# Kernel optimization log

Measured on AMD Instinct MI355X. Metric: run time of the kernel, lower is better.

## Reference

```python
import jax, jax.numpy as jnp
import numpy as np

GROUPS = 4
CHANNELS = 512
SCALE = 0.02


def setup_inputs() -> dict:
    key = jax.random.key(0)
    k_x, k_w1, k_w2, k_b1, k_b2 = jax.random.split(key, 5)
    d = CHANNELS // GROUPS
    x = jax.random.normal(k_x, (8, CHANNELS, 128, 128), dtype=jnp.float32)
    w1 = SCALE * jax.random.normal(k_w1, (2, GROUPS, d, d), dtype=jnp.float32)
    w2 = SCALE * jax.random.normal(k_w2, (2, GROUPS, d, d), dtype=jnp.float32)
    b1 = SCALE * jax.random.normal(k_b1, (2, GROUPS, d), dtype=jnp.float32)
    b2 = SCALE * jax.random.normal(k_b2, (2, GROUPS, d), dtype=jnp.float32)
    return {"x": x, "w1": w1, "w2": w2, "b1": b1, "b2": b2}


def reference(x, w1, w2, b1, b2):
    B, C, H, W = x.shape
    g = w1.shape[1]
    d = C // g
    # FFT over spatial dims; spectrum [B, C, H, W//2+1] complex
    spec = jnp.fft.rfft2(x, axes=(2, 3), norm="ortho")
    origin = spec
    out = spec.reshape(B, g, d, H, spec.shape[-1])  # B (g d) H Wf -> B g d H Wf
    xr, xi = out.real, out.imag

    def cmul(ar, ai, w, b):
        # grouped complex matmul over channel dim + bias
        or_ = (jnp.einsum("bkihw,kio->bkohw", ar, w[0])
               - jnp.einsum("bkihw,kio->bkohw", ai, w[1])
               + b[0][None, :, :, None, None])
        oi_ = (jnp.einsum("bkihw,kio->bkohw", ai, w[0])
               + jnp.einsum("bkihw,kio->bkohw", ar, w[1])
               + b[1][None, :, :, None, None])
        return or_, oi_

    o1r, o1i = cmul(xr, xi, w1, b1)
    o1r, o1i = jax.nn.relu(o1r), jax.nn.relu(o1i)
    o2r, o2i = cmul(o1r, o1i, w2, b2)

    out_c = (o2r + 1j * o2i).reshape(B, C, H, spec.shape[-1])
    out_c = out_c * origin
    return jnp.fft.irfft2(out_c, s=(H, W), axes=(2, 3), norm="ortho")
```

## Files before the change

kernel.cpp:

```cpp
#include <hip/hip_runtime.h>
#include <hip/hip_bf16.h>


#define NB    8
#define NC    512
#define NG    4
#define ND    128
#define NH    128
#define NW    128
#define NWF   65
#define NM    (NWF * NH)
#define INV_N 0.0078125f

typedef unsigned short ushortT;
typedef unsigned int uintT;
typedef __bf16 bf16x8 __attribute__((ext_vector_type(8)));
typedef float f32x4 __attribute__((ext_vector_type(4)));

__device__ __forceinline__ ushortT f2b(float f) {
    __hip_bfloat16 h = __float2bfloat16(f);
    return __builtin_bit_cast(ushortT, h);
}

__device__ __forceinline__ uintT pk2(float a, float b) {
    return (uintT)f2b(a) | ((uintT)f2b(b) << 16);
}
__device__ __forceinline__ float lo2f(uintT u) {
    return __builtin_bit_cast(float, u << 16);
}
__device__ __forceinline__ float hi2f(uintT u) {
    return __builtin_bit_cast(float, u & 0xffff0000u);
}

__device__ __forceinline__ int sigma(int n) {
    return ((n & 15) << 4) | ((n >> 4) & 7) | ((n & 128) >> 4);
}

__device__ __forceinline__ int bitrev7(int x) {
    return (int)(__brev((unsigned)x) >> 25);
}

__device__ __forceinline__ int IDX(int r, int c) {
    return (r << 7) + (c ^ (r & 15));
}

__device__ __forceinline__ float2 cmul(float2 a, float2 b) {
    return make_float2(a.x * b.x - a.y * b.y, a.x * b.y + a.y * b.x);
}

template <bool INV>
__device__ __forceinline__ void r4pass(float2* D, const float2* __restrict__ twg,
                                       int tid, int s) {
    const int h = 1 << s;
#pragma unroll
    for (int t = 0; t < 2; t++) {
        const int idx = t * 1024 + tid;
        const int rlo = idx & 15;
        const int gid = (idx >> 4) & 31;
        const int r = ((idx >> 9) << 4) | rlo;
        const int j = gid & (h - 1);
        const int base = ((gid >> s) << (s + 2)) + j;
        float2 t2 = twg[j << (5 - s)];
        float2 t1 = twg[j << (6 - s)];
        if (INV) { t1.y = -t1.y; t2.y = -t2.y; }
        float2 a = D[IDX(r, base)];
        float2 b = D[IDX(r, base + h)];
        float2 c = D[IDX(r, base + 2 * h)];
        float2 d = D[IDX(r, base + 3 * h)];
        float2 tb = cmul(t1, b), td = cmul(t1, d);
        float2 a1 = make_float2(a.x + tb.x, a.y + tb.y);
        float2 b1 = make_float2(a.x - tb.x, a.y - tb.y);
        float2 c1 = make_float2(c.x + td.x, c.y + td.y);
        float2 d1 = make_float2(c.x - td.x, c.y - td.y);
        float2 tc = cmul(t2, c1), ud = cmul(t2, d1);
        float2 rot = INV ? make_float2(-ud.y, ud.x) : make_float2(ud.y, -ud.x);
        D[IDX(r, base)]         = make_float2(a1.x + tc.x, a1.y + tc.y);
        D[IDX(r, base + h)]     = make_float2(b1.x + rot.x, b1.y + rot.y);
        D[IDX(r, base + 2 * h)] = make_float2(a1.x - tc.x, a1.y - tc.y);
        D[IDX(r, base + 3 * h)] = make_float2(b1.x - rot.x, b1.y - rot.y);
    }
    __syncthreads();
}

template <bool INV>
__device__ __forceinline__ void r2final(float2* D, const float2* __restrict__ twg,
                                        int tid) {
#pragma unroll
    for (int t = 0; t < 4; t++) {
        const int idx = t * 1024 + tid;
        const int rlo = idx & 15;
        const int j = (idx >> 4) & 63;
        const int r = ((idx >> 10) << 4) | rlo;
        float2 w = twg[j];
        if (INV) w.y = -w.y;
        float2 xl = D[IDX(r, j)];
        float2 xh = D[IDX(r, j + 64)];
        const float tr = w.x * xh.x - w.y * xh.y;
        const float ti = w.x * xh.y + w.y * xh.x;
        D[IDX(r, j)]      = make_float2(xl.x + tr, xl.y + ti);
        D[IDX(r, j + 64)] = make_float2(xl.x - tr, xl.y - ti);
    }
    __syncthreads();
}

template <bool INV>
__device__ __forceinline__ void fft64x128(float2* D, const float2* __restrict__ twg,
                                          int tid) {
    r4pass<INV>(D, twg, tid, 0);
    r4pass<INV>(D, twg, tid, 2);
    r4pass<INV>(D, twg, tid, 4);
    r2final<INV>(D, twg, tid);
}

__global__ __launch_bounds__(1024, 8) void k_fwd2d(const float* __restrict__ x,
                                                   uintT* __restrict__ s0,
                                                   const float2* __restrict__ twg) {
    __shared__ float2 D[8192];
    const int tid = threadIdx.x;
    const int bc = blockIdx.x;

    const float* xr = x + (size_t)bc * (NH * NW);
#pragma unroll
    for (int t = 0; t < 2; t++) {
        int i = t * 1024 + tid;
        int hp = i >> 5;
        int w0 = (i & 31) * 4;
        float4 a = *(const float4*)(xr + (size_t)(2 * hp) * NW + w0);
        float4 b = *(const float4*)(xr + (size_t)(2 * hp + 1) * NW + w0);
        D[IDX(hp, bitrev7(w0 + 0))] = make_float2(a.x, b.x);
        D[IDX(hp, bitrev7(w0 + 1))] = make_float2(a.y, b.y);
        D[IDX(hp, bitrev7(w0 + 2))] = make_float2(a.z, b.z);
        D[IDX(hp, bitrev7(w0 + 3))] = make_float2(a.w, b.w);
    }
    __syncthreads();
    fft64x128<false>(D, twg, tid);

    float2 ra[4], rb[4];
#pragma unroll
    for (int t = 0; t < 4; t++) {
        int i = t * 1024 + tid;
        int hp = i >> 6, j = i & 63;
        ra[t] = D[IDX(hp, j)];
        rb[t] = D[IDX(hp, j ? (128 - j) : 64)];
    }
    __syncthreads();
#pragma unroll
    for (int t = 0; t < 4; t++) {
        int i = t * 1024 + tid;
        int hp = i >> 6, j = i & 63;
        int c0 = bitrev7(2 * hp), c1 = bitrev7(2 * hp + 1);
        float2 a = ra[t], b = rb[t];
        if (j == 0) {
            D[IDX(0, c0)] = make_float2(a.x, b.x);
            D[IDX(0, c1)] = make_float2(a.y, b.y);
        } else {
            D[IDX(j, c0)] = make_float2(0.5f * (a.x + b.x), 0.5f * (a.y - b.y));
            D[IDX(j, c1)] = make_float2(0.5f * (a.y + b.y), 0.5f * (b.x - a.x));
        }
    }
    __syncthreads();
    fft64x128<false>(D, twg, tid);

    uintT* o = s0 + (size_t)bc * NM;
#pragma unroll
    for (int t = 0; t < 8; t++) {
        int i = t * 1024 + tid;
        int r = i >> 7, k = i & 127;
        if (r) {
            float2 v = D[IDX(r, k)];
            o[r * 128 + k] = pk2(v.x * INV_N, v.y * INV_N);
        } else {
            float2 ck = D[IDX(0, k)];
            float2 cm = D[IDX(0, (128 - k) & 127)];
            o[k] = pk2(0.5f * (ck.x + cm.x) * INV_N,
                       0.5f * (ck.y - cm.y) * INV_N);
            o[64 * 128 + k] = pk2(0.5f * (ck.y + cm.y) * INV_N,
                                  0.5f * (cm.x - ck.x) * INV_N);
        }
    }
}

__global__ __launch_bounds__(1024, 8) void k_inv2d(const uintT* __restrict__ y,
                                                   float* __restrict__ out,
                                                   const float2* __restrict__ twg) {
    __shared__ float2 D[8192];
    const int tid = threadIdx.x;
    const int bc = blockIdx.x;

    const uintT* Yb = y + (size_t)bc * NM;
#pragma unroll
    for (int t = 0; t < 2; t++) {
        int i = t * 1024 + tid;
        int r = i >> 5;
        int kq = (i & 31) * 4;
        if (r) {
            uint4 v = *(const uint4*)(Yb + r * 128 + kq);
            D[IDX(r, bitrev7(kq + 0))] = make_float2(lo2f(v.x), hi2f(v.x));
            D[IDX(r, bitrev7(kq + 1))] = make_float2(lo2f(v.y), hi2f(v.y));
            D[IDX(r, bitrev7(kq + 2))] = make_float2(lo2f(v.z), hi2f(v.z));
            D[IDX(r, bitrev7(kq + 3))] = make_float2(lo2f(v.w), hi2f(v.w));
        } else {
#pragma unroll
            for (int dw = 0; dw < 4; dw++) {
                int k = kq + dw;
                int m = (128 - k) & 127;
                uintT a = Yb[k],            am = Yb[m];
                uintT b = Yb[64 * 128 + k], bm = Yb[64 * 128 + m];
                float h0x = 0.5f * (lo2f(a) + lo2f(am)), h0y = 0.5f * (hi2f(a) - hi2f(am));
                float h6x = 0.5f * (lo2f(b) + lo2f(bm)), h6y = 0.5f * (hi2f(b) - hi2f(bm));
                D[IDX(0, bitrev7(k))] = make_float2(h0x - h6y, h0y + h6x);
            }
        }
    }
    __syncthreads();
    fft64x128<true>(D, twg, tid);

    float2 ra[4], rb[4];
#pragma unroll
    for (int t = 0; t < 4; t++) {
        int i = t * 1024 + tid;
        int hp = (i & 15) | (((i >> 10) & 3) << 4);
        int j  = ((i >> 4) & 3) | (((i >> 6) & 15) << 2);
        ra[t] = D[IDX(j, 2 * hp)];
        rb[t] = D[IDX(j, 2 * hp + 1)];
    }
    __syncthreads();
#pragma unroll
    for (int t = 0; t < 4; t++) {
        int i = t * 1024 + tid;
        int hp = (i & 15) | (((i >> 10) & 3) << 4);
        int j  = ((i >> 4) & 3) | (((i >> 6) & 15) << 2);
        float2 e = ra[t], f = rb[t];
        if (j == 0) {
            D[IDX(hp, bitrev7(0))]  = make_float2(e.x, f.x);
            D[IDX(hp, bitrev7(64))] = make_float2(e.y, f.y);
        } else {
            D[IDX(hp, bitrev7(j))]       = make_float2(e.x - f.y, e.y + f.x);
            D[IDX(hp, bitrev7(128 - j))] = make_float2(e.x + f.y, f.x - e.y);
        }
    }
    __syncthreads();
    fft64x128<true>(D, twg, tid);

    float* ob = out + (size_t)bc * (NH * NW);
#pragma unroll
    for (int t = 0; t < 8; t++) {
        int i = t * 1024 + tid;
        int hp = i >> 7, w = i & 127;
        float2 v = D[IDX(hp, w)];
        ob[(size_t)(2 * hp) * NW + w]     = v.x * INV_N;
        ob[(size_t)(2 * hp + 1) * NW + w] = v.y * INV_N;
    }
}

__global__ __launch_bounds__(256) void k_prep_w(const float* __restrict__ w1,
                                                const float* __restrict__ w2,
                                                ushortT* __restrict__ Wp,
                                                float2* __restrict__ twg) {
    if (blockIdx.x == 0 && threadIdx.x < 64) {
        float s, c;
        sincosf(-3.14159265358979323846f * (float)threadIdx.x / 64.0f, &s, &c);
        twg[threadIdx.x] = make_float2(c, s);
    }
    int idx = blockIdx.x * 256 + threadIdx.x;
    int k = idx & 255;
    int n = (idx >> 8) & 255;
    int g = (idx >> 16) & 3;
    int l = idx >> 18;
    const float* w = l ? w2 : w1;
    int kk = l ? sigma(k) : k;
    int ki = kk & 127, no = n & 127;
    float val;
    if (kk < 128) {
        val = (n < 128) ? w[((0 * NG + g) * ND + ki) * ND + no]
                        : w[((1 * NG + g) * ND + ki) * ND + no];
    } else {
        val = (n < 128) ? -w[((1 * NG + g) * ND + ki) * ND + no]
                        :  w[((0 * NG + g) * ND + ki) * ND + no];
    }
    Wp[((size_t)(l * NG + g) * 256 + n) * 256 + k] = f2b(val);
}

__global__ __launch_bounds__(512, 4) void k_gemm_fused(uintT* __restrict__ S,
                                                       const ushortT* __restrict__ Wp,
                                                       const float* __restrict__ B1,
                                                       const float* __restrict__ B2) {
    __shared__ unsigned char smem[65536];
    ushortT* Alds = (ushortT*)smem;
    ushortT* o1l  = (ushortT*)smem;
    float2*  E    = (float2*)smem;

    const int tid = threadIdx.x;
    const int mt = blockIdx.x, bk = blockIdx.y;
    const int g = bk & 3;
    const int m0 = mt * 128;
    const int lane = tid & 63, wid = tid >> 6;
    const int col = lane & 15, quad = lane >> 4;
    const int wm = wid & 1, wn = wid >> 1;

    uintT* Ab = S + (size_t)(bk * ND) * NM + m0;
    const ushortT* Wg1 = Wp + (size_t)g * 65536;
    const ushortT* Wg2 = Wp + (size_t)(NG + g) * 65536;

    f32x4 acc[4][4];
#pragma unroll
    for (int i = 0; i < 4; i++)
#pragma unroll
        for (int j = 0; j < 4; j++) acc[i][j] = f32x4{0.f, 0.f, 0.f, 0.f};

    for (int s = 0; s < 2; s++) {
        const int cs = s * 64;
        __syncthreads();
        {
            const int oct = tid >> 6;
            const int mp = (tid & 63) * 2;
            union { ushortT u[8]; uint4 v; } re0, re1, im0, im1;
#pragma unroll
            for (int j = 0; j < 8; j++) {
                const uint2 v = *(const uint2*)(Ab + (size_t)(cs + oct * 8 + j) * NM + mp);
                re0.u[j] = (ushortT)(v.x & 0xffffu); im0.u[j] = (ushortT)(v.x >> 16);
                re1.u[j] = (ushortT)(v.y & 0xffffu); im1.u[j] = (ushortT)(v.y >> 16);
            }
            *(uint4*)&Alds[(oct * 128 + mp) * 8] = re0.v;
            *(uint4*)&Alds[(oct * 128 + mp + 1) * 8] = re1.v;
            *(uint4*)&Alds[((8 + oct) * 128 + mp) * 8] = im0.v;
            *(uint4*)&Alds[((8 + oct) * 128 + mp + 1) * 8] = im1.v;
        }
        __syncthreads();
#pragma unroll
        for (int h = 0; h < 2; h++) {
            const int kbase = h * 128 + cs;
#pragma unroll
            for (int ksl = 0; ksl < 2; ksl++) {
                bf16x8 a[4];
#pragma unroll
                for (int mi = 0; mi < 4; mi++)
                    a[mi] = *(const bf16x8*)&Alds[((h * 8 + ksl * 4 + quad) * 128
                                                   + wm * 64 + mi * 16 + col) * 8];
#pragma unroll
                for (int ni = 0; ni < 4; ni++) {
                    const int n = wn * 64 + ni * 16 + col;
                    bf16x8 b = *(const bf16x8*)(Wg1 + (size_t)n * 256 + kbase
                                                + (ksl * 4 + quad) * 8);
#pragma unroll
                    for (int mi = 0; mi < 4; mi++)
                        acc[mi][ni] = __builtin_amdgcn_mfma_f32_16x16x32_bf16(
                            a[mi], b, acc[mi][ni], 0, 0, 0);
                }
            }
        }
    }

    float bR[4];
#pragma unroll
    for (int ni = 0; ni < 4; ni++) {
        const int n = wn * 64 + ni * 16 + col;
        bR[ni] = (n < 128) ? B1[g * ND + n] : B1[512 + g * ND + (n - 128)];
    }
    __syncthreads();
    {
        const int kq = col * 2 + (wn >> 1);
        const int xo = col & 7;
        const int pos = (wn & 1) * 4;
#pragma unroll
        for (int mi = 0; mi < 4; mi++)
#pragma unroll
            for (int r = 0; r < 4; r++) {
                const int ml = wm * 64 + mi * 16 + quad * 4 + r;
                union { ushortT u[4]; uint2 v; } pk;
#pragma unroll
                for (int ni = 0; ni < 4; ni++)
                    pk.u[ni] = f2b(fmaxf(acc[mi][ni][r] + bR[ni], 0.f));
                *(uint2*)&o1l[(kq * 128 + (ml ^ xo)) * 8 + pos] = pk.v;
            }
    }
    __syncthreads();

#pragma unroll
    for (int i = 0; i < 4; i++)
#pragma unroll
        for (int j = 0; j < 4; j++) acc[i][j] = f32x4{0.f, 0.f, 0.f, 0.f};

#pragma unroll
    for (int kqs = 0; kqs < 8; kqs++) {
        const int kq = kqs * 4 + quad;
        const int xo = (kq >> 1) & 7;
        bf16x8 a[4];
#pragma unroll
        for (int mi = 0; mi < 4; mi++)
            a[mi] = *(const bf16x8*)&o1l[(kq * 128 + ((wm * 64 + mi * 16 + col) ^ xo)) * 8];
#pragma unroll
        for (int ni = 0; ni < 4; ni++) {
            const int n = wn * 64 + ni * 16 + col;
            bf16x8 b = *(const bf16x8*)(Wg2 + (size_t)n * 256 + (size_t)kq * 8);
#pragma unroll
            for (int mi = 0; mi < 4; mi++)
                acc[mi][ni] = __builtin_amdgcn_mfma_f32_16x16x32_bf16(
                    a[mi], b, acc[mi][ni], 0, 0, 0);
        }
    }

    const int ri = wn >> 1;
#pragma unroll
    for (int p = 0; p < 4; p++) {
        __syncthreads();
        if ((wn & 1) == (p >> 1)) {
#pragma unroll
            for (int q2 = 0; q2 < 2; q2++) {
                const int nic = (p & 1) * 2 + q2;
                const int ch_l = q2 * 16 + col;
                const int ch = p * 32 + ch_l;
                const float bias = ri ? B2[512 + g * ND + ch] : B2[g * ND + ch];
#pragma unroll
                for (int mi = 0; mi < 4; mi++)
#pragma unroll
                    for (int r = 0; r < 4; r++) {
                        const int ml = wm * 64 + mi * 16 + quad * 4 + r;
                        ((float*)&E[ch_l * 129 + ml])[ri] = acc[mi][nic][r] + bias;
                    }
            }
        }
        __syncthreads();
#pragma unroll
        for (int j = 0; j < 8; j++) {
            const int idx = j * 512 + tid;
            const int ch_l = idx >> 7, ml = idx & 127;
            const float2 v = E[ch_l * 129 + ml];
            uintT* Yp = Ab + (size_t)(p * 32 + ch_l) * NM + ml;
            const uintT o = *Yp;
            const float ox = lo2f(o), oy = hi2f(o);
            *Yp = pk2(v.x * ox - v.y * oy, v.x * oy + v.y * ox);
        }
    }
}

extern "C" void kernel_launch(void* const* d_in, const int* in_sizes, int n_in,
                              void* d_out, int out_size, void* d_ws, size_t ws_size,
                              hipStream_t stream) {
    (void)in_sizes; (void)n_in; (void)out_size; (void)ws_size;
    const float* x  = (const float*)d_in[0];
    const float* w1 = (const float*)d_in[1];
    const float* w2 = (const float*)d_in[2];
    const float* b1 = (const float*)d_in[3];
    const float* b2 = (const float*)d_in[4];
    float* outp = (float*)d_out;

    uintT* buf1 = (uintT*)d_ws;
    char*  ws2  = (char*)d_ws + (size_t)NB * NC * NM * sizeof(float2);
    ushortT* Wp  = (ushortT*)(ws2 + (size_t)144 * 1024 * 1024);
    float2* twg  = (float2*)((char*)Wp + (size_t)1048576);

    k_prep_w<<<dim3(2048), 256, 0, stream>>>(w1, w2, Wp, twg);
    k_fwd2d<<<dim3(NB * NC), 1024, 0, stream>>>(x, buf1, twg);
    k_gemm_fused<<<dim3(NM / 128, NB * NG), 512, 0, stream>>>(buf1, Wp, b1, b2);
    k_inv2d<<<dim3(NB * NC), 1024, 0, stream>>>(buf1, outp, twg);
}
```

Measured before the change: 772.0 us.

## Prefetch activations, double-buffer weight loads, and hoist origin loads in fused GEMM

The fused spectral GEMM kernel now loads both halves of the A tile from global memory into registers up front. It double-buffers the weight fragments so the next k-slice's weights load while the current MFMAs run. In the epilogue, the origin spectrum values are read before the LDS staging barrier so their global latency overlaps the accumulator writes. The change targets exposed global-load latency, at the cost of higher register pressure under launch_bounds(512,4), which could cause spills or lower occupancy.

```diff
diff --git a/kernel.cpp b/kernel.cpp
--- a/kernel.cpp
+++ b/kernel.cpp
@@ -281,6 +281,26 @@
     Wp[((size_t)(l * NG + g) * 256 + n) * 256 + k] = f2b(val);
 }
 
+__device__ __forceinline__ void ldw4(bf16x8* arr, const ushortT* __restrict__ Wg,
+                                     int nbase, int koff) {
+#pragma unroll
+    for (int ni = 0; ni < 4; ni++)
+        arr[ni] = *(const bf16x8*)(Wg + (size_t)(nbase + ni * 16) * 256 + koff);
+}
+
+__device__ __forceinline__ void stageA(ushortT* Alds, const uint2* a, int oct, int mp) {
+    union { ushortT u[8]; uint4 v; } re0, re1, im0, im1;
+#pragma unroll
+    for (int j = 0; j < 8; j++) {
+        re0.u[j] = (ushortT)(a[j].x & 0xffffu); im0.u[j] = (ushortT)(a[j].x >> 16);
+        re1.u[j] = (ushortT)(a[j].y & 0xffffu); im1.u[j] = (ushortT)(a[j].y >> 16);
+    }
+    *(uint4*)&Alds[(oct * 128 + mp) * 8]       = re0.v;
+    *(uint4*)&Alds[(oct * 128 + mp + 1) * 8]   = re1.v;
+    *(uint4*)&Alds[((8 + oct) * 128 + mp) * 8]     = im0.v;
+    *(uint4*)&Alds[((8 + oct) * 128 + mp + 1) * 8] = im1.v;
+}
+
 __global__ __launch_bounds__(512, 4) void k_gemm_fused(uintT* __restrict__ S,
                                                        const ushortT* __restrict__ Wp,
                                                        const float* __restrict__ B1,
@@ -297,59 +317,25 @@
     const int lane = tid & 63, wid = tid >> 6;
     const int col = lane & 15, quad = lane >> 4;
     const int wm = wid & 1, wn = wid >> 1;
+    const int nbase = wn * 64 + col;
+    const int q8 = quad * 8;
 
     uintT* Ab = S + (size_t)(bk * ND) * NM + m0;
     const ushortT* Wg1 = Wp + (size_t)g * 65536;
     const ushortT* Wg2 = Wp + (size_t)(NG + g) * 65536;
 
-    f32x4 acc[4][4];
-#pragma unroll
-    for (int i = 0; i < 4; i++)
-#pragma unroll
-        for (int j = 0; j < 4; j++) acc[i][j] = f32x4{0.f, 0.f, 0.f, 0.f};
-
-    for (int s = 0; s < 2; s++) {
-        const int cs = s * 64;
-        __syncthreads();
-        {
-            const int oct = tid >> 6;
-            const int mp = (tid & 63) * 2;
-            union { ushortT u[8]; uint4 v; } re0, re1, im0, im1;
-#pragma unroll
-            for (int j = 0; j < 8; j++) {
-                const uint2 v = *(const uint2*)(Ab + (size_t)(cs + oct * 8 + j) * NM + mp);
-                re0.u[j] = (ushortT)(v.x & 0xffffu); im0.u[j] = (ushortT)(v.x >> 16);
-                re1.u[j] = (ushortT)(v.y & 0xffffu); im1.u[j] = (ushortT)(v.y >> 16);
-            }
-            *(uint4*)&Alds[(oct * 128 + mp) * 8] = re0.v;
-            *(uint4*)&Alds[(oct * 128 + mp + 1) * 8] = re1.v;
-            *(uint4*)&Alds[((8 + oct) * 128 + mp) * 8] = im0.v;
-            *(uint4*)&Alds[((8 + oct) * 128 + mp + 1) * 8] = im1.v;
-        }
-        __syncthreads();
-#pragma unroll
-        for (int h = 0; h < 2; h++) {
-            const int kbase = h * 128 + cs;
-#pragma unroll
-            for (int ksl = 0; ksl < 2; ksl++) {
-                bf16x8 a[4];
-#pragma unroll
-                for (int mi = 0; mi < 4; mi++)
-                    a[mi] = *(const bf16x8*)&Alds[((h * 8 + ksl * 4 + quad) * 128
-                                                   + wm * 64 + mi * 16 + col) * 8];
-#pragma unroll
-                for (int ni = 0; ni < 4; ni++) {
-                    const int n = wn * 64 + ni * 16 + col;
-                    bf16x8 b = *(const bf16x8*)(Wg1 + (size_t)n * 256 + kbase
-                                                + (ksl * 4 + quad) * 8);
-#pragma unroll
-                    for (int mi = 0; mi < 4; mi++)
-                        acc[mi][ni] = __builtin_amdgcn_mfma_f32_16x16x32_bf16(
-                            a[mi], b, acc[mi][ni], 0, 0, 0);
-                }
-            }
-        }
-    }
+    uint2 a0[8], a1[8];
+    const int oct = tid >> 6;
+    const int mp = (tid & 63) * 2;
+#pragma unroll
+    for (int j = 0; j < 8; j++)
+        a0[j] = *(const uint2*)(Ab + (size_t)(oct * 8 + j) * NM + mp);
+#pragma unroll
+    for (int j = 0; j < 8; j++)
+        a1[j] = *(const uint2*)(Ab + (size_t)(64 + oct * 8 + j) * NM + mp);
+
+    bf16x8 bw[2][4];
+    ldw4(bw[0], Wg1, nbase, q8);
 
     float bR[4];
 #pragma unroll
@@ -357,6 +343,61 @@
         const int n = wn * 64 + ni * 16 + col;
         bR[ni] = (n < 128) ? B1[g * ND + n] : B1[512 + g * ND + (n - 128)];
     }
+
+    f32x4 acc[4][4];
+#pragma unroll
+    for (int i = 0; i < 4; i++)
+#pragma unroll
+        for (int j = 0; j < 4; j++) acc[i][j] = f32x4{0.f, 0.f, 0.f, 0.f};
+
+    stageA(Alds, a0, oct, mp);
+    __syncthreads();
+
+#pragma unroll
+    for (int b = 0; b < 4; b++) {
+        const int h = (b >> 1) & 1, ksl = b & 1;
+        bf16x8 av[4];
+#pragma unroll
+        for (int mi = 0; mi < 4; mi++)
+            av[mi] = *(const bf16x8*)&Alds[((h * 8 + ksl * 4 + quad) * 128
+                                            + wm * 64 + mi * 16 + col) * 8];
+        const int nb = b + 1;
+        ldw4(bw[nb & 1], Wg1, nbase,
+             (((nb >> 1) & 1) * 128 + (nb >> 2) * 64 + (nb & 1) * 32) + q8);
+#pragma unroll
+        for (int ni = 0; ni < 4; ni++)
+#pragma unroll
+            for (int mi = 0; mi < 4; mi++)
+                acc[mi][ni] = __builtin_amdgcn_mfma_f32_16x16x32_bf16(
+                    av[mi], bw[b & 1][ni], acc[mi][ni], 0, 0, 0);
+    }
+    __syncthreads();
+    stageA(Alds, a1, oct, mp);
+    __syncthreads();
+
+#pragma unroll
+    for (int b = 4; b < 8; b++) {
+        const int h = (b >> 1) & 1, ksl = b & 1;
+        bf16x8 av[4];
+#pragma unroll
+        for (int mi = 0; mi < 4; mi++)
+            av[mi] = *(const bf16x8*)&Alds[((h * 8 + ksl * 4 + quad) * 128
+                                            + wm * 64 + mi * 16 + col) * 8];
+        if (b < 7) {
+            const int nb = b + 1;
+            ldw4(bw[nb & 1], Wg1, nbase,
+                 (((nb >> 1) & 1) * 128 + (nb >> 2) * 64 + (nb & 1) * 32) + q8);
+        } else {
+            ldw4(bw[0], Wg2, nbase, q8);
+        }
+#pragma unroll
+        for (int ni = 0; ni < 4; ni++)
+#pragma unroll
+            for (int mi = 0; mi < 4; mi++)
+                acc[mi][ni] = __builtin_amdgcn_mfma_f32_16x16x32_bf16(
+                    av[mi], bw[b & 1][ni], acc[mi][ni], 0, 0, 0);
+    }
+
     __syncthreads();
     {
         const int kq = col * 2 + (wn >> 1);
@@ -382,28 +423,33 @@
         for (int j = 0; j < 4; j++) acc[i][j] = f32x4{0.f, 0.f, 0.f, 0.f};
 
 #pragma unroll
-    for (int kqs = 0; kqs < 8; kqs++) {
-        const int kq = kqs * 4 + quad;
+    for (int b = 0; b < 8; b++) {
+        const int kq = b * 4 + quad;
         const int xo = (kq >> 1) & 7;
-        bf16x8 a[4];
+        bf16x8 av[4];
 #pragma unroll
         for (int mi = 0; mi < 4; mi++)
-            a[mi] = *(const bf16x8*)&o1l[(kq * 128 + ((wm * 64 + mi * 16 + col) ^ xo)) * 8];
-#pragma unroll
-        for (int ni = 0; ni < 4; ni++) {
-            const int n = wn * 64 + ni * 16 + col;
-            bf16x8 b = *(const bf16x8*)(Wg2 + (size_t)n * 256 + (size_t)kq * 8);
+            av[mi] = *(const bf16x8*)&o1l[(kq * 128 + ((wm * 64 + mi * 16 + col) ^ xo)) * 8];
+        if (b < 7)
+            ldw4(bw[(b + 1) & 1], Wg2, nbase, (b + 1) * 32 + q8);
+#pragma unroll
+        for (int ni = 0; ni < 4; ni++)
 #pragma unroll
             for (int mi = 0; mi < 4; mi++)
                 acc[mi][ni] = __builtin_amdgcn_mfma_f32_16x16x32_bf16(
-                    a[mi], b, acc[mi][ni], 0, 0, 0);
-        }
+                    av[mi], bw[b & 1][ni], acc[mi][ni], 0, 0, 0);
     }
 
     const int ri = wn >> 1;
+    const int eml = tid & 127;
+    const int ecl = tid >> 7;
 #pragma unroll
     for (int p = 0; p < 4; p++) {
         __syncthreads();
+        uintT og[8];
+#pragma unroll
+        for (int j = 0; j < 8; j++)
+            og[j] = Ab[(size_t)(p * 32 + j * 4 + ecl) * NM + eml];
         if ((wn & 1) == (p >> 1)) {
 #pragma unroll
             for (int q2 = 0; q2 < 2; q2++) {
@@ -423,13 +469,11 @@
         __syncthreads();
 #pragma unroll
         for (int j = 0; j < 8; j++) {
-            const int idx = j * 512 + tid;
-            const int ch_l = idx >> 7, ml = idx & 127;
-            const float2 v = E[ch_l * 129 + ml];
-            uintT* Yp = Ab + (size_t)(p * 32 + ch_l) * NM + ml;
-            const uintT o = *Yp;
-            const float ox = lo2f(o), oy = hi2f(o);
-            *Yp = pk2(v.x * ox - v.y * oy, v.x * oy + v.y * ox);
+            const int ch_l = j * 4 + ecl;
+            const float2 v = E[ch_l * 129 + eml];
+            const float ox = lo2f(og[j]), oy = hi2f(og[j]);
+            Ab[(size_t)(p * 32 + ch_l) * NM + eml] =
+                pk2(v.x * ox - v.y * oy, v.x * oy + v.y * ox);
         }
     }
 }
```

Measured after the change: 781.3 us. Within noise of the previous version (+1.2%).

## Give each wavefront its own FFT rows to drop per-pass block barriers

Applied to the files above, without the earlier changes.

The work mapping inside the 64x128 shared-memory FFT changes so each 64-lane wavefront owns four complete rows across all radix passes. A row's butterflies then only touch data held by the same wavefront, so the three __syncthreads between passes are removed, leaving one barrier after the whole FFT. The LDS index swizzle gains an extra XOR term to limit bank conflicts under the new access pattern. The change relies on wavefront lockstep execution and LDS ordering inside a wave being enough for correctness without explicit barriers.

```diff
diff --git a/kernel.cpp b/kernel.cpp
--- a/kernel.cpp
+++ b/kernel.cpp
@@ -41,7 +41,7 @@
 }
 
 __device__ __forceinline__ int IDX(int r, int c) {
-    return (r << 7) + (c ^ (r & 15));
+    return (r << 7) + (c ^ (r & 15) ^ ((r & 3) << 2));
 }
 
 __device__ __forceinline__ float2 cmul(float2 a, float2 b) {
@@ -50,14 +50,12 @@
 
 template <bool INV>
 __device__ __forceinline__ void r4pass(float2* D, const float2* __restrict__ twg,
-                                       int tid, int s) {
+                                       int lane, int rbase, int s) {
     const int h = 1 << s;
+    const int r = rbase + (lane >> 4);
 #pragma unroll
     for (int t = 0; t < 2; t++) {
-        const int idx = t * 1024 + tid;
-        const int rlo = idx & 15;
-        const int gid = (idx >> 4) & 31;
-        const int r = ((idx >> 9) << 4) | rlo;
+        const int gid = (lane & 15) + 16 * t;
         const int j = gid & (h - 1);
         const int base = ((gid >> s) << (s + 2)) + j;
         float2 t2 = twg[j << (5 - s)];
@@ -79,18 +77,15 @@
         D[IDX(r, base + 2 * h)] = make_float2(a1.x - tc.x, a1.y - tc.y);
         D[IDX(r, base + 3 * h)] = make_float2(b1.x - rot.x, b1.y - rot.y);
     }
-    __syncthreads();
 }
 
 template <bool INV>
 __device__ __forceinline__ void r2final(float2* D, const float2* __restrict__ twg,
-                                        int tid) {
+                                        int lane, int rbase) {
+    const int r = rbase + (lane >> 4);
 #pragma unroll
     for (int t = 0; t < 4; t++) {
-        const int idx = t * 1024 + tid;
-        const int rlo = idx & 15;
-        const int j = (idx >> 4) & 63;
-        const int r = ((idx >> 10) << 4) | rlo;
+        const int j = (lane & 15) + 16 * t;
         float2 w = twg[j];
         if (INV) w.y = -w.y;
         float2 xl = D[IDX(r, j)];
@@ -100,16 +95,17 @@
         D[IDX(r, j)]      = make_float2(xl.x + tr, xl.y + ti);
         D[IDX(r, j + 64)] = make_float2(xl.x - tr, xl.y - ti);
     }
-    __syncthreads();
 }
 
 template <bool INV>
 __device__ __forceinline__ void fft64x128(float2* D, const float2* __restrict__ twg,
                                           int tid) {
-    r4pass<INV>(D, twg, tid, 0);
-    r4pass<INV>(D, twg, tid, 2);
-    r4pass<INV>(D, twg, tid, 4);
-    r2final<INV>(D, twg, tid);
+    const int lane = tid & 63;
+    const int rbase = (tid >> 6) * 4;
+    r4pass<INV>(D, twg, lane, rbase, 0);
+    r4pass<INV>(D, twg, lane, rbase, 2);
+    r4pass<INV>(D, twg, lane, rbase, 4);
+    r2final<INV>(D, twg, lane, rbase);
 }
 
 __global__ __launch_bounds__(1024, 8) void k_fwd2d(const float* __restrict__ x,
@@ -134,6 +130,7 @@
     }
     __syncthreads();
     fft64x128<false>(D, twg, tid);
+    __syncthreads();
 
     float2 ra[4], rb[4];
 #pragma unroll
@@ -160,6 +157,7 @@
     }
     __syncthreads();
     fft64x128<false>(D, twg, tid);
+    __syncthreads();
 
     uintT* o = s0 + (size_t)bc * NM;
 #pragma unroll
@@ -214,6 +212,7 @@
     }
     __syncthreads();
     fft64x128<true>(D, twg, tid);
+    __syncthreads();
 
     float2 ra[4], rb[4];
 #pragma unroll
@@ -241,6 +240,7 @@
     }
     __syncthreads();
     fft64x128<true>(D, twg, tid);
+    __syncthreads();
 
     float* ob = out + (size_t)bc * (NH * NW);
 #pragma unroll
```

Measured after the change: 844.4 us. 1.09x slower.
